# Kernel optimization log

Hardware: AMD Instinct MI355X
Metric: run time of the kernel (lower is better)

## Reference

```python
import jax, jax.numpy as jnp
import numpy as np

NUM_WORDS = 32768
MAX_CHARS = 20
NUM_CHARS = 128
EMB = 64
H = 128   # word_hidden_size (per direction)
C = 128   # context_vector_size


def setup_inputs() -> dict:
    key = jax.random.key(0)
    ks = jax.random.split(key, 16)
    s = 1.0 / np.sqrt(H)  # torch GRU default init scale
    u = lambda k, shape, sc: jax.random.uniform(k, shape, jnp.float32, -sc, sc)
    inp = {
        'padded_char_tensor': jax.random.randint(ks[0], (NUM_WORDS, MAX_CHARS), 0, NUM_CHARS),
        'sequence_lens': jax.random.randint(ks[1], (NUM_WORDS,), 1, MAX_CHARS + 1),
        'emb': jax.random.normal(ks[2], (NUM_CHARS, EMB), jnp.float32),
        # forward-direction GRU params (torch layout: gates r,z,n stacked)
        'Wih_f': u(ks[3], (3 * H, EMB), s),
        'Whh_f': u(ks[4], (3 * H, H), s),
        'bih_f': u(ks[5], (3 * H,), s),
        'bhh_f': u(ks[6], (3 * H,), s),
        # backward-direction GRU params
        'Wih_b': u(ks[7], (3 * H, EMB), s),
        'Whh_b': u(ks[8], (3 * H, H), s),
        'bih_b': u(ks[9], (3 * H,), s),
        'bhh_b': u(ks[10], (3 * H,), s),
        # word_projection Linear(2H -> C)
        'Wp': u(ks[11], (C, 2 * H), 1.0 / np.sqrt(2 * H)),
        'bp': u(ks[12], (C,), 1.0 / np.sqrt(2 * H)),
        # word context vector [C, 1]
        'ctx': u(ks[13], (C, 1), 0.1),
    }
    return inp


def _gru_dir(x_proj, Whh, bhh):
    # x_proj: [B, T, 3H] precomputed input projection; scan over T
    Hn = Whh.shape[1]
    def step(h, xt):
        hp = h @ Whh.T + bhh
        r = jax.nn.sigmoid(xt[:, :Hn] + hp[:, :Hn])
        z = jax.nn.sigmoid(xt[:, Hn:2 * Hn] + hp[:, Hn:2 * Hn])
        n = jnp.tanh(xt[:, 2 * Hn:] + r * hp[:, 2 * Hn:])
        h = (1.0 - z) * n + z * h
        return h, h
    h0 = jnp.zeros((x_proj.shape[0], Hn), x_proj.dtype)
    _, ys = jax.lax.scan(step, h0, x_proj.transpose(1, 0, 2))
    return ys.transpose(1, 0, 2)  # [B, T, H]


def _rev_within(x, lens):
    # reverse each sequence within its valid length (packed-sequence semantics)
    T = x.shape[1]
    t = jnp.arange(T)[None, :]
    idx = jnp.where(t < lens[:, None], lens[:, None] - 1 - t, t)
    return jnp.take_along_axis(x, idx[:, :, None], axis=1)


def _forward(chars, lens, emb, Wih_f, Whh_f, bih_f, bhh_f,
             Wih_b, Whh_b, bih_b, bhh_b, Wp, bp, ctx):
    x = emb[chars]  # [B, T, EMB]; dropout_p=0 -> identity
    mask = (jnp.arange(x.shape[1])[None, :] < lens[:, None])  # [B, T]
    out_f = _gru_dir(x @ Wih_f.T + bih_f, Whh_f, bhh_f)
    xb = _rev_within(x, lens)
    out_b = _gru_dir(xb @ Wih_b.T + bih_b, Whh_b, bhh_b)
    out_b = _rev_within(out_b, lens)
    # pad_packed_sequence zero-pads beyond each length
    out = jnp.concatenate([out_f, out_b], axis=-1) * mask[:, :, None]  # [B, T, 2H]
    proj = jnp.tanh(out @ Wp.T + bp)                # [B, T, C]
    scores = jnp.einsum('btc,c->bt', proj, ctx[:, 0])
    att = jax.nn.softmax(scores, axis=-1)           # softmax over char positions
    return jnp.einsum('bt,btd->bd', att, out)       # [B, 2H]


def reference(padded_char_tensor, sequence_lens, emb, Wih_f, Whh_f, bih_f, bhh_f,
              Wih_b, Whh_b, bih_b, bhh_b, Wp, bp, ctx):
    return _forward(padded_char_tensor, sequence_lens, emb, Wih_f, Whh_f, bih_f,
                    bhh_f, Wih_b, Whh_b, bih_b, bhh_b, Wp, bp, ctx)
```

## Files before the change

kernel.cpp:

```cpp
#include <hip/hip_runtime.h>
#include <hip/hip_bf16.h>
#include <stdint.h>


typedef unsigned short u16;
typedef float f32x4 __attribute__((ext_vector_type(4)));
typedef __bf16 bf16x8 __attribute__((ext_vector_type(8)));

#if __has_builtin(__builtin_amdgcn_exp2f)
#define EXP2F(x) __builtin_amdgcn_exp2f(x)
#else
#define EXP2F(x) exp2f(x)
#endif
#if __has_builtin(__builtin_amdgcn_rcpf)
#define RCPF(x) __builtin_amdgcn_rcpf(x)
#else
#define RCPF(x) (1.0f / (x))
#endif

#define LOG2E 1.4426950408889634f

__device__ __forceinline__ u16 f2b(float f) {
  uint32_t u = __builtin_bit_cast(uint32_t, f);
  u = u + 0x7FFFu + ((u >> 16) & 1u);
  return (u16)(u >> 16);
}
__device__ __forceinline__ float b2f(u16 s) {
  uint32_t u = ((uint32_t)s) << 16;
  return __builtin_bit_cast(float, u);
}
__device__ __forceinline__ float fast_sig(float x) {
  return RCPF(1.0f + EXP2F(-LOG2E * x));
}
__device__ __forceinline__ float fast_tanh(float x) {
  return 1.0f - 2.0f * RCPF(EXP2F(2.0f * LOG2E * x) + 1.0f);
}

__global__ void prep_kernel(
    const float* __restrict__ emb,
    const float* __restrict__ wih_f, const float* __restrict__ bih_f,
    const float* __restrict__ wih_b, const float* __restrict__ bih_b,
    const float* __restrict__ whh_f_in, const float* __restrict__ whh_b_in,
    const float* __restrict__ wp_in,
    u16* __restrict__ xpj_f, u16* __restrict__ xpj_b,
    u16* __restrict__ whhf, u16* __restrict__ whhb, u16* __restrict__ wpf) {
  int gid = blockIdx.x * 256 + threadIdx.x;
  if (blockIdx.x < 1024) {
    int d = gid >> 17;
    int r = gid & 131071;
    int c = r >> 10;
    int r2 = r & 1023;
    int j2 = r2 >> 9;
    int r3 = r2 & 511;
    int w16 = r3 >> 2;
    int slot = r3 & 3;
    float v = 0.f;
    if (slot < 3) {
      int gate = slot * 128 + (w16 >> 4) * 32 + j2 * 16 + (w16 & 15);
      const float* wih = d ? wih_b : wih_f;
      const float* bih = d ? bih_b : bih_f;
      const float4* e4 = (const float4*)(emb + c * 64);
      const float4* w4 = (const float4*)(wih + gate * 64);
      float s = 0.f;
#pragma unroll
      for (int e = 0; e < 16; e++) {
        float4 a = e4[e], b = w4[e];
        s += a.x * b.x + a.y * b.y + a.z * b.z + a.w * b.w;
      }
      v = s + bih[gate];
    }
    (d ? xpj_b : xpj_f)[r] = f2b(v);
  } else if (blockIdx.x < 1072) {
    int idx = gid - 1024 * 256;
    int d = (idx >= 6144) ? 1 : 0;
    int r = idx - d * 6144;
    int lane = r & 63, kt = (r >> 6) & 3, nt = r >> 8;
    int n = nt * 16 + (lane & 15);
    int k0 = kt * 32 + (lane >> 4) * 8;
    const float* w = d ? whh_b_in : whh_f_in;
    u16* o = (d ? whhb : whhf) + r * 8;
    for (int j = 0; j < 8; j++) o[j] = f2b(w[n * 128 + k0 + j]);
  } else {
    int idx = gid - 1072 * 256;
    if (idx < 4096) {
      int lane = idx & 63, kt = (idx >> 6) & 7, nt = idx >> 9;
      int n = nt * 16 + (lane & 15);
      int k0 = kt * 32 + (lane >> 4) * 8;
      u16* o = wpf + idx * 8;
      for (int j = 0; j < 8; j++) o[j] = f2b(wp_in[n * 256 + k0 + j]);
    }
  }
}

__global__ void sort_zero(int* __restrict__ bins) {
  if (threadIdx.x < 32) bins[threadIdx.x] = 0;
}
__global__ void sort_hist(const int* __restrict__ lens, int* __restrict__ bins) {
  __shared__ int hcnt[32];
  int tid = threadIdx.x;
  if (tid < 32) hcnt[tid] = 0;
  __syncthreads();
  int gid = blockIdx.x * 256 + tid;
  int l = lens[gid] & 31;
  atomicAdd(&hcnt[l], 1);
  __syncthreads();
  if (tid < 32 && hcnt[tid]) atomicAdd(&bins[tid], hcnt[tid]);
}
__global__ void sort_scan(const int* __restrict__ bins, int* __restrict__ offsw,
                          const float* __restrict__ bp,
                          const float* __restrict__ ctx,
                          float* __restrict__ c0out) {
  if (threadIdx.x == 0 && blockIdx.x == 0) {
    int off = 0;
    for (int l = 0; l < 32; l++) {
      offsw[l] = off;
      off += bins[l];
    }
    float c0 = 0.f;
    for (int c = 0; c < 128; c++) c0 += fast_tanh(bp[c]) * ctx[c];
    *c0out = c0;
  }
}
__global__ void sort_scat(const int* __restrict__ lens, int* __restrict__ offsw,
                          int* __restrict__ perm) {
  __shared__ int lcnt[32];
  __shared__ int lbase[32];
  int tid = threadIdx.x;
  if (tid < 32) lcnt[tid] = 0;
  __syncthreads();
  int gid = blockIdx.x * 256 + tid;
  int l = lens[gid] & 31;
  int lr = atomicAdd(&lcnt[l], 1);
  __syncthreads();
  if (tid < 32) lbase[tid] = lcnt[tid] ? atomicAdd(&offsw[tid], lcnt[tid]) : 0;
  __syncthreads();
  perm[lbase[l] + lr] = gid;
}

__global__ __launch_bounds__(512, 4) void gru_kernel(
    const int* __restrict__ chars, const int* __restrict__ lens,
    const int* __restrict__ perm,
    const u16* __restrict__ xpj_f, const u16* __restrict__ xpj_b,
    const u16* __restrict__ whhf, const u16* __restrict__ whhb,
    const float* __restrict__ bhh_f, const float* __restrict__ bhh_b,
    u16* __restrict__ hf, u16* __restrict__ hb, int word_off, int nbd) {
  const int bid = blockIdx.x;
  const int dir = bid & 1;
  const int wg = nbd - 1 - (bid >> 1);
  const int tid = threadIdx.x;

  __shared__ int perm_s[16];
  __shared__ unsigned char lens_s[16];
  __shared__ unsigned char chars_s[320];
  __shared__ u16 h_s[2][2048];

  if (tid < 16) {
    int p = perm[word_off + wg * 16 + tid];
    perm_s[tid] = p;
    lens_s[tid] = (unsigned char)lens[p];
  }
  for (int i = tid; i < 1024; i += 512) ((uint32_t*)h_s[0])[i] = 0u;
  __syncthreads();

  for (int i = tid; i < 320; i += 512) {
    int w = i & 15, s = i >> 4;
    int L = lens_s[w];
    int t = dir ? ((s < L) ? (L - 1 - s) : s) : s;
    chars_s[s * 16 + w] = (unsigned char)chars[perm_s[w] * 20 + t];
  }

  const u16* xp = dir ? xpj_b : xpj_f;
  const u16* whh = dir ? whhb : whhf;
  const float* bhh = dir ? bhh_b : bhh_f;
  u16* hout = (dir ? hb : hf) + (size_t)wg * 16 * 2560;

  const int wv = tid >> 6, ln = tid & 63, col = ln & 15, grp = ln >> 4;
  const int j2 = wv & 1, hg = wv >> 1;

  bf16x8 Bf[3][4];
#pragma unroll
  for (int cls = 0; cls < 3; cls++) {
    int nt = cls * 8 + hg * 2 + j2;
#pragma unroll
    for (int kt = 0; kt < 4; kt++)
      Bf[cls][kt] = *(const bf16x8*)(whh + (((nt * 4 + kt) * 64 + ln) << 3));
  }

  float bh[3];
#pragma unroll
  for (int cls = 0; cls < 3; cls++)
    bh[cls] = bhh[cls * 128 + hg * 32 + j2 * 16 + col];

  __syncthreads();

  const int Lmax = lens_s[15];

  const int swd = tid >> 5;
  const int k4 = (tid & 31) << 2;
  const int skt = k4 >> 5;
  const int slan = swd | (((k4 >> 3) & 3) << 4);
  const int sslot = k4 & 7;
  const int sL = lens_s[swd];

  float h[4] = {0.f, 0.f, 0.f, 0.f};

  uint2 xq[4];
#pragma unroll
  for (int r = 0; r < 4; r++) {
    int c = chars_s[grp * 4 + r];
    xq[r] = *(const uint2*)(xp + ((((c << 1) + j2) << 7) + (hg << 4) + col) * 4);
  }

  for (int s = 0; s < Lmax; s++) {
    const u16* hcur = h_s[s & 1];
    u16* hnxt = h_s[(s + 1) & 1];

    uint2 xc[4];
#pragma unroll
    for (int r = 0; r < 4; r++) xc[r] = xq[r];
    if (s + 1 < Lmax) {
#pragma unroll
      for (int r = 0; r < 4; r++) {
        int c = chars_s[(s + 1) * 16 + grp * 4 + r];
        xq[r] =
            *(const uint2*)(xp + ((((c << 1) + j2) << 7) + (hg << 4) + col) * 4);
      }
    }

    f32x4 acc[3];
#pragma unroll
    for (int cls = 0; cls < 3; cls++)
      acc[cls] = (f32x4){bh[cls], bh[cls], bh[cls], bh[cls]};
#pragma unroll
    for (int kt = 0; kt < 4; kt++) {
      bf16x8 Af = *(const bf16x8*)(hcur + ((kt * 64 + ln) << 3));
#pragma unroll
      for (int cls = 0; cls < 3; cls++)
        acc[cls] =
            __builtin_amdgcn_mfma_f32_16x16x32_bf16(Af, Bf[cls][kt], acc[cls], 0, 0, 0);
    }

#pragma unroll
    for (int r = 0; r < 4; r++) {
      const u16* e = (const u16*)&xc[r];
      float rr = fast_sig(b2f(e[0]) + acc[0][r]);
      float zz = fast_sig(b2f(e[1]) + acc[1][r]);
      float nn = fast_tanh(b2f(e[2]) + rr * acc[2][r]);
      float hn = (1.f - zz) * nn + zz * h[r];
      h[r] = hn;
      int lane_a = (grp * 4 + r) | ((j2 * 2 + (col >> 3)) << 4);
      hnxt[((hg * 64 + lane_a) << 3) + (col & 7)] = f2b(hn);
    }
    __syncthreads();

    if (s < sL) {
      int tdst = dir ? (sL - 1 - s) : s;
      uint2 v = *(const uint2*)(hnxt + ((skt * 64 + slan) << 3) + sslot);
      *(uint2*)(hout + ((size_t)swd * 20 + tdst) * 128 + k4) = v;
    }
  }
}

__global__ __launch_bounds__(256, 2) void attn_kernel(
    const u16* __restrict__ hf, const u16* __restrict__ hb,
    const u16* __restrict__ wpf,
    const float* __restrict__ bp, const float* __restrict__ ctx,
    const int* __restrict__ perm, const int* __restrict__ lens,
    const float* __restrict__ c0p,
    float* __restrict__ out, int word_off) {
  const int blk = gridDim.x - 1 - blockIdx.x;
  const int lw0 = blk * 16;

  __shared__ u16 ot_s[4096];
  __shared__ float part_s[4][16];
  __shared__ int perm_s[16];
  __shared__ unsigned char lens_s[16];

  const int tid = threadIdx.x;
  const int wv = tid >> 6, ln = tid & 63, col = ln & 15, grp = ln >> 4;
  const int sw = tid >> 4;
  const int seg = tid & 15;

  if (tid < 16) {
    int p = perm[word_off + lw0 + tid];
    perm_s[tid] = p;
    lens_s[tid] = (unsigned char)lens[p];
  }
  __syncthreads();
  const int Lmax = lens_s[15];
  const int Lw = lens_s[sw];

  float bpv[2], ctxv[2];
#pragma unroll
  for (int n = 0; n < 2; n++) {
    int nt = wv + n * 4;
    bpv[n] = bp[nt * 16 + col];
    ctxv[n] = ctx[nt * 16 + col];
  }

  float facc[16];
#pragma unroll
  for (int i = 0; i < 16; i++) facc[i] = 0.f;
  float mrun = -3.0e38f, drun = 0.f;

  const u16* srcbase =
      ((seg < 8) ? hf : hb) + (size_t)(lw0 + sw) * 2560 + (seg & 7) * 16;

  uint4 vn[2];
#pragma unroll
  for (int q = 0; q < 2; q++) vn[q] = *(const uint4*)(srcbase + q * 8);

  for (int t = 0; t < Lmax; t++) {
    uint4 v[2];
    v[0] = vn[0];
    v[1] = vn[1];

#pragma unroll
    for (int q = 0; q < 2; q++) {
      int idx = seg * 2 + q;
      int kt = idx >> 2;
      int lane_a = sw | ((idx & 3) << 4);
      *(uint4*)(ot_s + ((kt * 64 + lane_a) << 3)) = v[q];
    }
    if (t + 1 < Lmax) {
      const u16* src = srcbase + (t + 1) * 128;
#pragma unroll
      for (int q = 0; q < 2; q++) vn[q] = *(const uint4*)(src + q * 8);
    }
    __syncthreads();

    f32x4 acc[2];
#pragma unroll
    for (int n = 0; n < 2; n++) acc[n] = (f32x4){bpv[n], bpv[n], bpv[n], bpv[n]};

#pragma unroll
    for (int kt = 0; kt < 8; kt++) {
      bf16x8 Af = *(const bf16x8*)(ot_s + ((kt * 64 + ln) << 3));
#pragma unroll
      for (int n = 0; n < 2; n++) {
        int nt = wv + n * 4;
        bf16x8 Bf = *(const bf16x8*)(wpf + (((nt * 8 + kt) * 64 + ln) << 3));
        acc[n] = __builtin_amdgcn_mfma_f32_16x16x32_bf16(Af, Bf, acc[n], 0, 0, 0);
      }
    }

#pragma unroll
    for (int r = 0; r < 4; r++) {
      float p = fast_tanh(acc[0][r]) * ctxv[0] + fast_tanh(acc[1][r]) * ctxv[1];
      p += __shfl_xor(p, 1, 64);
      p += __shfl_xor(p, 2, 64);
      p += __shfl_xor(p, 4, 64);
      p += __shfl_xor(p, 8, 64);
      if (col == 0) part_s[wv][grp * 4 + r] = p;
    }
    __syncthreads();

    float sc = part_s[0][sw] + part_s[1][sw] + part_s[2][sw] + part_s[3][sw];

    if (t < Lw) {
      float mnew = fmaxf(mrun, sc);
      float scale = EXP2F(LOG2E * (mrun - mnew));
      float e = EXP2F(LOG2E * (sc - mnew));
      drun = drun * scale + e;
      mrun = mnew;
#pragma unroll
      for (int q = 0; q < 2; q++) {
        const u16* pv = (const u16*)&v[q];
#pragma unroll
        for (int j = 0; j < 8; j++)
          facc[q * 8 + j] = facc[q * 8 + j] * scale + e * b2f(pv[j]);
      }
    }
  }

  drun += (float)(20 - Lw) * EXP2F(LOG2E * (*c0p - mrun));

  float inv = RCPF(drun);
  float* dst = out + (size_t)perm_s[sw] * 256 + seg * 16;
#pragma unroll
  for (int i = 0; i < 4; i++) {
    float4 o = make_float4(facc[i * 4] * inv, facc[i * 4 + 1] * inv,
                           facc[i * 4 + 2] * inv, facc[i * 4 + 3] * inv);
    *(float4*)(dst + i * 4) = o;
  }
}

extern "C" void kernel_launch(void* const* d_in, const int* in_sizes, int n_in,
                              void* d_out, int out_size, void* d_ws, size_t ws_size,
                              hipStream_t stream) {
  const int* chars = (const int*)d_in[0];
  const int* lens = (const int*)d_in[1];
  const float* emb = (const float*)d_in[2];
  const float* wih_f = (const float*)d_in[3];
  const float* whh_f = (const float*)d_in[4];
  const float* bih_f = (const float*)d_in[5];
  const float* bhh_f = (const float*)d_in[6];
  const float* wih_b = (const float*)d_in[7];
  const float* whh_b = (const float*)d_in[8];
  const float* bih_b = (const float*)d_in[9];
  const float* bhh_b = (const float*)d_in[10];
  const float* wp = (const float*)d_in[11];
  const float* bp = (const float*)d_in[12];
  const float* ctx = (const float*)d_in[13];
  float* outp = (float*)d_out;

  uint8_t* ws = (uint8_t*)d_ws;
  u16* xpj_f = (u16*)(ws + 0);
  u16* xpj_b = (u16*)(ws + 262144);
  u16* whhf = (u16*)(ws + 524288);
  u16* whhb = (u16*)(ws + 622592);
  u16* wpf = (u16*)(ws + 720896);
  int* bins = (int*)(ws + 786432);
  int* offsw = (int*)(ws + 786560);
  float* c0p = (float*)(ws + 786688);
  int* permp = (int*)(ws + 786752);
  const size_t H_OFF = 1048576;

  prep_kernel<<<1088, 256, 0, stream>>>(emb, wih_f, bih_f, wih_b, bih_b, whh_f,
                                        whh_b, wp, xpj_f, xpj_b, whhf, whhb, wpf);
  sort_zero<<<1, 64, 0, stream>>>(bins);
  sort_hist<<<128, 256, 0, stream>>>(lens, bins);
  sort_scan<<<1, 64, 0, stream>>>(bins, offsw, bp, ctx, c0p);
  sort_scat<<<128, 256, 0, stream>>>(lens, offsw, permp);

  const size_t per_word = 20 * 128 * 2 * 2;
  size_t avail = (ws_size > H_OFF) ? (ws_size - H_OFF) : 0;
  int maxw = (int)(avail / per_word) & ~63;
  if (maxw > 32768) maxw = 32768;
  if (maxw < 64) maxw = 64;

  for (int done = 0; done < 32768;) {
    int nw = (32768 - done < maxw) ? (32768 - done) : maxw;
    u16* hfp = (u16*)(ws + H_OFF);
    u16* hbp = hfp + (size_t)nw * 2560;
    int nbd = nw / 16;
    gru_kernel<<<2 * nbd, 512, 0, stream>>>(chars, lens, permp, xpj_f, xpj_b,
                                            whhf, whhb, bhh_f, bhh_b, hfp, hbp,
                                            done, nbd);
    attn_kernel<<<nw / 16, 256, 0, stream>>>(hfp, hbp, wpf, bp, ctx, permp,
                                             lens, c0p, outp, done);
    done += nw;
  }
}
```

Before: 262.8 us.

## Transpose GRU MFMA orientation and prefold exp scales and biases into weights

```diff
diff --git a/kernel.cpp b/kernel.cpp
--- a/kernel.cpp
+++ b/kernel.cpp
@@ -29,59 +29,71 @@
   uint32_t u = ((uint32_t)s) << 16;
   return __builtin_bit_cast(float, u);
 }
-__device__ __forceinline__ float fast_sig(float x) {
-  return RCPF(1.0f + EXP2F(-LOG2E * x));
-}
 __device__ __forceinline__ float fast_tanh(float x) {
   return 1.0f - 2.0f * RCPF(EXP2F(2.0f * LOG2E * x) + 1.0f);
+}
+__device__ __forceinline__ uint32_t cvtpk(float a, float b) {
+  uint32_t r;
+  asm("v_cvt_pk_bf16_f32 %0, %1, %2" : "=v"(r) : "v"(a), "v"(b));
+  return r;
 }
 
 __global__ void prep_kernel(
     const float* __restrict__ emb,
     const float* __restrict__ wih_f, const float* __restrict__ bih_f,
     const float* __restrict__ wih_b, const float* __restrict__ bih_b,
+    const float* __restrict__ bhh_f, const float* __restrict__ bhh_b,
     const float* __restrict__ whh_f_in, const float* __restrict__ whh_b_in,
     const float* __restrict__ wp_in,
-    u16* __restrict__ xpj_f, u16* __restrict__ xpj_b,
+    float* __restrict__ xpf_f, float* __restrict__ xpf_b,
     u16* __restrict__ whhf, u16* __restrict__ whhb, u16* __restrict__ wpf) {
   int gid = blockIdx.x * 256 + threadIdx.x;
-  if (blockIdx.x < 1024) {
-    int d = gid >> 17;
-    int r = gid & 131071;
-    int c = r >> 10;
-    int r2 = r & 1023;
-    int j2 = r2 >> 9;
-    int r3 = r2 & 511;
-    int w16 = r3 >> 2;
-    int slot = r3 & 3;
-    float v = 0.f;
-    if (slot < 3) {
-      int gate = slot * 128 + (w16 >> 4) * 32 + j2 * 16 + (w16 & 15);
-      const float* wih = d ? wih_b : wih_f;
-      const float* bih = d ? bih_b : bih_f;
-      const float4* e4 = (const float4*)(emb + c * 64);
-      const float4* w4 = (const float4*)(wih + gate * 64);
-      float s = 0.f;
-#pragma unroll
-      for (int e = 0; e < 16; e++) {
-        float4 a = e4[e], b = w4[e];
-        s += a.x * b.x + a.y * b.y + a.z * b.z + a.w * b.w;
-      }
-      v = s + bih[gate];
-    }
-    (d ? xpj_b : xpj_f)[r] = f2b(v);
-  } else if (blockIdx.x < 1072) {
-    int idx = gid - 1024 * 256;
+  if (blockIdx.x < 384) {
+    int e = gid;
+    int d = (e >= 49152) ? 1 : 0;
+    int r = e - d * 49152;
+    int j = r & 3;
+    int e2 = r >> 2;
+    int cls = e2 % 3;
+    int e3 = e2 / 3;
+    int grp = e3 & 3;
+    int e4 = e3 >> 2;
+    int wv = e4 & 7;
+    int c = e4 >> 3;
+    int row = cls * 128 + wv * 16 + grp * 4 + j;
+    const float* wih = d ? wih_b : wih_f;
+    const float* bih = d ? bih_b : bih_f;
+    const float* bhh = d ? bhh_b : bhh_f;
+    const float4* e4p = (const float4*)(emb + c * 64);
+    const float4* w4p = (const float4*)(wih + row * 64);
+    float s = 0.f;
+#pragma unroll
+    for (int q = 0; q < 16; q++) {
+      float4 a = e4p[q], b = w4p[q];
+      s += a.x * b.x + a.y * b.y + a.z * b.z + a.w * b.w;
+    }
+    s += bih[row];
+    float scale;
+    if (cls < 2) {
+      s += bhh[row];
+      scale = -LOG2E;
+    } else {
+      scale = 2.0f * LOG2E;
+    }
+    (d ? xpf_b : xpf_f)[r] = s * scale;
+  } else if (blockIdx.x < 432) {
+    int idx = gid - 384 * 256;
     int d = (idx >= 6144) ? 1 : 0;
     int r = idx - d * 6144;
     int lane = r & 63, kt = (r >> 6) & 3, nt = r >> 8;
+    float scale = (nt < 16) ? -LOG2E : 2.0f * LOG2E;
     int n = nt * 16 + (lane & 15);
     int k0 = kt * 32 + (lane >> 4) * 8;
     const float* w = d ? whh_b_in : whh_f_in;
     u16* o = (d ? whhb : whhf) + r * 8;
-    for (int j = 0; j < 8; j++) o[j] = f2b(w[n * 128 + k0 + j]);
+    for (int j = 0; j < 8; j++) o[j] = f2b(w[n * 128 + k0 + j] * scale);
   } else {
-    int idx = gid - 1072 * 256;
+    int idx = gid - 432 * 256;
     if (idx < 4096) {
       int lane = idx & 63, kt = (idx >> 6) & 7, nt = idx >> 9;
       int n = nt * 16 + (lane & 15);
@@ -140,7 +152,7 @@
 __global__ __launch_bounds__(512, 4) void gru_kernel(
     const int* __restrict__ chars, const int* __restrict__ lens,
     const int* __restrict__ perm,
-    const u16* __restrict__ xpj_f, const u16* __restrict__ xpj_b,
+    const float* __restrict__ xpf_f, const float* __restrict__ xpf_b,
     const u16* __restrict__ whhf, const u16* __restrict__ whhb,
     const float* __restrict__ bhh_f, const float* __restrict__ bhh_b,
     u16* __restrict__ hf, u16* __restrict__ hb, int word_off, int nbd) {
@@ -151,7 +163,7 @@
 
   __shared__ int perm_s[16];
   __shared__ unsigned char lens_s[16];
-  __shared__ unsigned char chars_s[320];
+  __shared__ int coff_s[320];
   __shared__ u16 h_s[2][2048];
 
   if (tid < 16) {
@@ -159,106 +171,103 @@
     perm_s[tid] = p;
     lens_s[tid] = (unsigned char)lens[p];
   }
-  for (int i = tid; i < 1024; i += 512) ((uint32_t*)h_s[0])[i] = 0u;
-  __syncthreads();
-
+  for (int i = tid; i < 1024; i += 512) ((uint32_t*)h_s)[i] = 0u;
+  __syncthreads();
   for (int i = tid; i < 320; i += 512) {
     int w = i & 15, s = i >> 4;
     int L = lens_s[w];
     int t = dir ? ((s < L) ? (L - 1 - s) : s) : s;
-    chars_s[s * 16 + w] = (unsigned char)chars[perm_s[w] * 20 + t];
-  }
-
-  const u16* xp = dir ? xpj_b : xpj_f;
+    coff_s[s * 16 + w] = chars[perm_s[w] * 20 + t] * 384;
+  }
+
+  const float* xp = dir ? xpf_b : xpf_f;
   const u16* whh = dir ? whhb : whhf;
   const float* bhh = dir ? bhh_b : bhh_f;
   u16* hout = (dir ? hb : hf) + (size_t)wg * 16 * 2560;
 
-  const int wv = tid >> 6, ln = tid & 63, col = ln & 15, grp = ln >> 4;
-  const int j2 = wv & 1, hg = wv >> 1;
-
-  bf16x8 Bf[3][4];
+  const int wv = tid >> 6, ln = tid & 63, word = ln & 15, grp = ln >> 4;
+  const float* xpt = xp + (wv * 4 + grp) * 12;
+
+  bf16x8 Wf[3][4];
 #pragma unroll
   for (int cls = 0; cls < 3; cls++) {
-    int nt = cls * 8 + hg * 2 + j2;
+    int nt = cls * 8 + wv;
 #pragma unroll
     for (int kt = 0; kt < 4; kt++)
-      Bf[cls][kt] = *(const bf16x8*)(whh + (((nt * 4 + kt) * 64 + ln) << 3));
-  }
-
-  float bh[3];
-#pragma unroll
-  for (int cls = 0; cls < 3; cls++)
-    bh[cls] = bhh[cls * 128 + hg * 32 + j2 * 16 + col];
+      Wf[cls][kt] = *(const bf16x8*)(whh + (((nt * 4 + kt) * 64 + ln) << 3));
+  }
+  float4 bhn = *(const float4*)(bhh + 256 + wv * 16 + grp * 4);
+  bhn.x *= 2.0f * LOG2E; bhn.y *= 2.0f * LOG2E;
+  bhn.z *= 2.0f * LOG2E; bhn.w *= 2.0f * LOG2E;
 
   __syncthreads();
 
   const int Lmax = lens_s[15];
 
+  const int hw_off =
+      (((wv >> 1) * 64) + (word | (((wv & 1) * 2 + (grp >> 1)) << 4))) * 16 +
+      (grp & 1) * 8;
   const int swd = tid >> 5;
   const int k4 = (tid & 31) << 2;
-  const int skt = k4 >> 5;
-  const int slan = swd | (((k4 >> 3) & 3) << 4);
-  const int sslot = k4 & 7;
   const int sL = lens_s[swd];
-
-  float h[4] = {0.f, 0.f, 0.f, 0.f};
-
-  uint2 xq[4];
-#pragma unroll
-  for (int r = 0; r < 4; r++) {
-    int c = chars_s[grp * 4 + r];
-    xq[r] = *(const uint2*)(xp + ((((c << 1) + j2) << 7) + (hg << 4) + col) * 4);
-  }
-
-  for (int s = 0; s < Lmax; s++) {
-    const u16* hcur = h_s[s & 1];
-    u16* hnxt = h_s[(s + 1) & 1];
-
-    uint2 xc[4];
-#pragma unroll
-    for (int r = 0; r < 4; r++) xc[r] = xq[r];
-    if (s + 1 < Lmax) {
-#pragma unroll
-      for (int r = 0; r < 4; r++) {
-        int c = chars_s[(s + 1) * 16 + grp * 4 + r];
-        xq[r] =
-            *(const uint2*)(xp + ((((c << 1) + j2) << 7) + (hg << 4) + col) * 4);
-      }
-    }
-
-    f32x4 acc[3];
-#pragma unroll
-    for (int cls = 0; cls < 3; cls++)
-      acc[cls] = (f32x4){bh[cls], bh[cls], bh[cls], bh[cls]};
-#pragma unroll
-    for (int kt = 0; kt < 4; kt++) {
-      bf16x8 Af = *(const bf16x8*)(hcur + ((kt * 64 + ln) << 3));
-#pragma unroll
-      for (int cls = 0; cls < 3; cls++)
-        acc[cls] =
-            __builtin_amdgcn_mfma_f32_16x16x32_bf16(Af, Bf[cls][kt], acc[cls], 0, 0, 0);
-    }
-
-#pragma unroll
-    for (int r = 0; r < 4; r++) {
-      const u16* e = (const u16*)&xc[r];
-      float rr = fast_sig(b2f(e[0]) + acc[0][r]);
-      float zz = fast_sig(b2f(e[1]) + acc[1][r]);
-      float nn = fast_tanh(b2f(e[2]) + rr * acc[2][r]);
-      float hn = (1.f - zz) * nn + zz * h[r];
-      h[r] = hn;
-      int lane_a = (grp * 4 + r) | ((j2 * 2 + (col >> 3)) << 4);
-      hnxt[((hg * 64 + lane_a) << 3) + (col & 7)] = f2b(hn);
-    }
-    __syncthreads();
-
-    if (s < sL) {
-      int tdst = dir ? (sL - 1 - s) : s;
-      uint2 v = *(const uint2*)(hnxt + ((skt * 64 + slan) << 3) + sslot);
-      *(uint2*)(hout + ((size_t)swd * 20 + tdst) * 128 + k4) = v;
-    }
-  }
+  const int hs_off =
+      (((k4 >> 5) * 64) + (swd | (((k4 >> 3) & 3) << 4))) * 16 + (k4 & 7) * 2;
+
+  char* hsb = (char*)h_s;
+
+  float hreg[4] = {0.f, 0.f, 0.f, 0.f};
+  f32x4 xA0, xA1, xA2, xB0, xB1, xB2;
+  {
+    int off = coff_s[word];
+    xA0 = *(const f32x4*)(xpt + off);
+    xA1 = *(const f32x4*)(xpt + off + 4);
+    xA2 = *(const f32x4*)(xpt + off + 8);
+  }
+
+#define GSTEP(S, PAR, XC0, XC1, XC2, XN0, XN1, XN2)                           \
+  {                                                                           \
+    if ((S) + 1 < Lmax) {                                                     \
+      int off = coff_s[((S) + 1) * 16 + word];                                \
+      XN0 = *(const f32x4*)(xpt + off);                                       \
+      XN1 = *(const f32x4*)(xpt + off + 4);                                   \
+      XN2 = *(const f32x4*)(xpt + off + 8);                                   \
+    }                                                                         \
+    f32x4 a0 = (f32x4){0.f, 0.f, 0.f, 0.f};                                   \
+    f32x4 a1 = (f32x4){0.f, 0.f, 0.f, 0.f};                                   \
+    f32x4 a2 = (f32x4){bhn.x, bhn.y, bhn.z, bhn.w};                           \
+    _Pragma("unroll")                                                         \
+    for (int kt = 0; kt < 4; kt++) {                                          \
+      bf16x8 Hf =                                                             \
+          *(const bf16x8*)(hsb + (PAR) * 4096 + ((kt * 64 + ln) << 4));       \
+      a0 = __builtin_amdgcn_mfma_f32_16x16x32_bf16(Wf[0][kt], Hf, a0, 0, 0, 0); \
+      a1 = __builtin_amdgcn_mfma_f32_16x16x32_bf16(Wf[1][kt], Hf, a1, 0, 0, 0); \
+      a2 = __builtin_amdgcn_mfma_f32_16x16x32_bf16(Wf[2][kt], Hf, a2, 0, 0, 0); \
+    }                                                                         \
+    _Pragma("unroll")                                                         \
+    for (int r = 0; r < 4; r++) {                                             \
+      float rr = RCPF(1.0f + EXP2F(XC0[r] + a0[r]));                          \
+      float zz = RCPF(1.0f + EXP2F(XC1[r] + a1[r]));                          \
+      float na = fmaf(rr, a2[r], XC2[r]);                                     \
+      float nn = fmaf(-2.0f, RCPF(EXP2F(na) + 1.0f), 1.0f);                   \
+      hreg[r] = fmaf(zz, hreg[r] - nn, nn);                                   \
+    }                                                                         \
+    {                                                                         \
+      uint2 pk = make_uint2(cvtpk(hreg[0], hreg[1]), cvtpk(hreg[2], hreg[3]));\
+      *(uint2*)(hsb + ((PAR) ^ 1) * 4096 + hw_off) = pk;                      \
+    }                                                                         \
+    __syncthreads();                                                          \
+    if ((S) < sL) {                                                           \
+      int tdst = dir ? (sL - 1 - (S)) : (S);                                  \
+      uint2 v = *(const uint2*)(hsb + ((PAR) ^ 1) * 4096 + hs_off);           \
+      *(uint2*)(hout + ((size_t)swd * 20 + tdst) * 128 + k4) = v;             \
+    }                                                                         \
+  }
+
+  for (int s = 0; s < Lmax; s += 2) {
+    GSTEP(s, 0, xA0, xA1, xA2, xB0, xB1, xB2);
+    if (s + 1 < Lmax) GSTEP(s + 1, 1, xB0, xB1, xB2, xA0, xA1, xA2);
+  }
+#undef GSTEP
 }
 
 __global__ __launch_bounds__(256, 2) void attn_kernel(
@@ -405,19 +414,20 @@
   float* outp = (float*)d_out;
 
   uint8_t* ws = (uint8_t*)d_ws;
-  u16* xpj_f = (u16*)(ws + 0);
-  u16* xpj_b = (u16*)(ws + 262144);
-  u16* whhf = (u16*)(ws + 524288);
-  u16* whhb = (u16*)(ws + 622592);
-  u16* wpf = (u16*)(ws + 720896);
-  int* bins = (int*)(ws + 786432);
-  int* offsw = (int*)(ws + 786560);
-  float* c0p = (float*)(ws + 786688);
-  int* permp = (int*)(ws + 786752);
+  float* xpf_f = (float*)(ws + 0);
+  float* xpf_b = (float*)(ws + 196608);
+  u16* whhf = (u16*)(ws + 393216);
+  u16* whhb = (u16*)(ws + 491520);
+  u16* wpf = (u16*)(ws + 589824);
+  int* bins = (int*)(ws + 655360);
+  int* offsw = (int*)(ws + 655488);
+  float* c0p = (float*)(ws + 655616);
+  int* permp = (int*)(ws + 655680);
   const size_t H_OFF = 1048576;
 
-  prep_kernel<<<1088, 256, 0, stream>>>(emb, wih_f, bih_f, wih_b, bih_b, whh_f,
-                                        whh_b, wp, xpj_f, xpj_b, whhf, whhb, wpf);
+  prep_kernel<<<448, 256, 0, stream>>>(emb, wih_f, bih_f, wih_b, bih_b, bhh_f,
+                                       bhh_b, whh_f, whh_b, wp, xpf_f, xpf_b,
+                                       whhf, whhb, wpf);
   sort_zero<<<1, 64, 0, stream>>>(bins);
   sort_hist<<<128, 256, 0, stream>>>(lens, bins);
   sort_scan<<<1, 64, 0, stream>>>(bins, offsw, bp, ctx, c0p);
@@ -434,7 +444,7 @@
     u16* hfp = (u16*)(ws + H_OFF);
     u16* hbp = hfp + (size_t)nw * 2560;
     int nbd = nw / 16;
-    gru_kernel<<<2 * nbd, 512, 0, stream>>>(chars, lens, permp, xpj_f, xpj_b,
+    gru_kernel<<<2 * nbd, 512, 0, stream>>>(chars, lens, permp, xpf_f, xpf_b,
                                             whhf, whhb, bhh_f, bhh_b, hfp, hbp,
                                             done, nbd);
     attn_kernel<<<nw / 16, 256, 0, stream>>>(hfp, hbp, wpf, bp, ctx, permp,
```

Measured after the change: 276.3 us. +5.1%, slower.
